# Kernel tuning notes

Measured on AMD Instinct MI355X. Metric: run time of the kernel, lower is better.

## Reference

```python
import jax, jax.numpy as jnp
import numpy as np

B, F, U, O, A, H = 8192, 1024, 512, 3, 6, 4  # batch, features, nb_units, nb_opponents, actions, heads
HD = U // H  # head dim


def setup_inputs() -> dict:
    key = jax.random.key(0)
    ks = jax.random.split(key, 12)
    s = 0.02
    rn = lambda k, shape: jax.random.normal(k, shape, jnp.float32) * s
    return {
        "features": jax.random.normal(ks[0], (B, F), jnp.float32),
        # agent latent Linear
        "W_al": rn(ks[1], (U, F)), "b_al": jnp.zeros((U,), jnp.float32),
        # MultiheadAttention in_proj (q,k,v stacked) and out_proj
        "W_in": rn(ks[2], (3 * U, U)), "b_in": jnp.zeros((3 * U,), jnp.float32),
        "W_out": rn(ks[3], (U, U)), "b_out": jnp.zeros((U,), jnp.float32),
        # agent head / policy / value
        "W_ah": rn(ks[4], (U, 2 * U)), "b_ah": jnp.zeros((U,), jnp.float32),
        "W_ap": rn(ks[5], (A, U)), "b_ap": jnp.zeros((A,), jnp.float32),
        "W_av": rn(ks[6], (1, U)), "b_av": jnp.zeros((1,), jnp.float32),
        # per-opponent stacks: latent, head, policy, value
        "W_ol": rn(ks[7], (O, U, F)), "b_ol": jnp.zeros((O, U), jnp.float32),
        "W_oh": rn(ks[8], (O, U, U)), "b_oh": jnp.zeros((O, U), jnp.float32),
        "W_op": rn(ks[9], (O, A, U)), "b_op": jnp.zeros((O, A), jnp.float32),
        "W_ov": rn(ks[10], (O, 1, U)), "b_ov": jnp.zeros((O, 1), jnp.float32),
    }


def reference(features, W_al, b_al, W_in, b_in, W_out, b_out, W_ah, b_ah,
              W_ap, b_ap, W_av, b_av, W_ol, b_ol, W_oh, b_oh, W_op, b_op, W_ov, b_ov):
    elu = jax.nn.elu
    # agent + per-opponent latents (per-opponent linears as one grouped GEMM)
    agent_latent = elu(features @ W_al.T + b_al)                                # [B,U]
    opp_lat = elu(jnp.einsum('bf,ouf->obu', features, W_ol) + b_ol[:, None, :])  # [O,B,U]

    # torch.nn.MultiheadAttention: query=[1,B,U] (agent), key=value=[O,B,U] (opponents)
    Wq, Wk, Wv = W_in[:U], W_in[U:2 * U], W_in[2 * U:]
    bq, bk, bv = b_in[:U], b_in[U:2 * U], b_in[2 * U:]
    q = (agent_latent @ Wq.T + bq).reshape(B, H, HD) * (1.0 / np.sqrt(HD))      # [B,H,HD]
    k = (jnp.einsum('obu,vu->obv', opp_lat, Wk) + bk).reshape(O, B, H, HD)
    v = (jnp.einsum('obu,vu->obv', opp_lat, Wv) + bv).reshape(O, B, H, HD)
    scores = jnp.einsum('bhd,obhd->bho', q, k)                                  # [B,H,O]
    w = jax.nn.softmax(scores, axis=-1)
    attn = jnp.einsum('bho,obhd->bhd', w, v).reshape(B, U)
    attn_out = attn @ W_out.T + b_out                                           # [B,U]
    opponents_influences = w.mean(axis=1)                                       # [B,O] (avg over heads)

    # agent head / policy / value
    cat = jnp.concatenate([agent_latent, attn_out], axis=1)                     # [B,2U]
    agent_head = elu(cat @ W_ah.T + b_ah)
    agent_policy = agent_head @ W_ap.T + b_ap                                   # [B,A]
    agent_value = agent_head @ W_av.T + b_av                                    # [B,1]

    # per-opponent head / policy / value (grouped GEMMs)
    opp_heads = elu(jnp.einsum('obu,ovu->obv', opp_lat, W_oh) + b_oh[:, None, :])  # [O,B,U]
    opponents_policies = jnp.einsum('obu,oau->boa', opp_heads, W_op) + b_op[None]   # [B,O,A]
    opponents_values = jnp.einsum('obu,ocu->boc', opp_heads, W_ov) + b_ov[None]     # [B,O,1]

    return (agent_policy, agent_value, opponents_policies, opponents_values, opponents_influences)
```

## Files before the change

kernel.cpp:

```cpp
#include <hip/hip_runtime.h>

typedef unsigned short u16;
typedef __bf16 bf16x8 __attribute__((ext_vector_type(8)));
typedef float f32x4 __attribute__((ext_vector_type(4)));

#define Bsz 8192
#define Fdim 1024
#define Udim 512
#define Odim 3
#define Adim 6
#define Hdim 4

#define OFF_FEAT   0
#define OFF_WAL    8388608
#define OFF_WIN    10485760
#define OFF_WOUT   11272192
#define OFF_WAH    11534336
#define OFF_WOH    12058624
#define OFF_LAT    12845056
#define OFF_Q      29622272
#define OFF_KV     33816576
#define OFF_OPH    67371008
#define OFF_WOUTT  79953920
#define OFF_WCOMB  80216064
#define OFF_BAHC   80478208
#define OFF_ZB     80479232

#define OUT_AP 0
#define OUT_AV 49152
#define OUT_OP 57344
#define OUT_OV 204800
#define OUT_IN 229376

__device__ __forceinline__ u16 f2bf(float f) {
  return __builtin_bit_cast(u16, (__bf16)f);
}
__device__ __forceinline__ float bf2f(u16 u) {
  return (float)__builtin_bit_cast(__bf16, u);
}

__device__ __forceinline__ void gload16(const u16* g, u16* s) {
  __builtin_amdgcn_global_load_lds(
      (const __attribute__((address_space(1))) unsigned int*)g,
      (__attribute__((address_space(3))) unsigned int*)s, 16, 0, 0);
}

#define CV_E0 2097152
#define CV_E1 2228224
#define CV_E2 2621440
#define CV_E3 2818048
#define CV_E4 2883584
#define CV_E5 3014656
#define CV_E6 3211264
__global__ __launch_bounds__(256) void convert_all(
    const float* __restrict__ f, const float* __restrict__ wal,
    const float* __restrict__ wol, const float* __restrict__ win,
    const float* __restrict__ wout, const float* __restrict__ wah,
    const float* __restrict__ woh, u16* __restrict__ dst,
    u16* __restrict__ woutT, float* __restrict__ bahc,
    const float* __restrict__ bout_f, const float* __restrict__ bah_f,
    float* __restrict__ zb) {
  if (blockIdx.x >= 12608) {
    const int wave = threadIdx.x >> 6, lane = threadIdx.x & 63;
    const int jbase = (blockIdx.x - 12608) * 8 + wave * 2;
#pragma unroll
    for (int t = 0; t < 2; ++t) {
      const int j = jbase + t;
      float s = 0.f;
#pragma unroll
      for (int c = 0; c < 8; ++c)
        s += wah[j * 1024 + 512 + c * 64 + lane] * bout_f[c * 64 + lane];
#pragma unroll
      for (int d = 32; d; d >>= 1) s += __shfl_xor(s, d, 64);
      if (lane == 0) bahc[j] = bah_f[j] + s;
    }
    return;
  }
  if (blockIdx.x >= 12544) {
    const int bid = blockIdx.x - 12544;
    if (bid == 0) {
      zb[threadIdx.x] = 0.f;
      zb[threadIdx.x + 256] = 0.f;
    }
    __shared__ float tile[64][65];
    const int bx = bid & 7, byy = bid >> 3;
    const int v0 = byy * 64, u0 = bx * 64;
#pragma unroll
    for (int it = 0; it < 16; ++it) {
      int idx = it * 256 + threadIdx.x;
      int r = idx >> 6, c = idx & 63;
      tile[r][c] = wout[(v0 + r) * 512 + u0 + c];
    }
    __syncthreads();
#pragma unroll
    for (int it = 0; it < 16; ++it) {
      int idx = it * 256 + threadIdx.x;
      int r = idx >> 6, c = idx & 63;
      woutT[(u0 + r) * 512 + v0 + c] = f2bf(tile[c][r]);
    }
    return;
  }
  int i = blockIdx.x * 256 + threadIdx.x;
  const float* src;
  int base;
  if (i < CV_E0)      { src = f;    base = 0; }
  else if (i < CV_E1) { src = wal;  base = CV_E0; }
  else if (i < CV_E2) { src = wol;  base = CV_E1; }
  else if (i < CV_E3) { src = win;  base = CV_E2; }
  else if (i < CV_E4) { src = wout; base = CV_E3; }
  else if (i < CV_E5) { src = wah;  base = CV_E4; }
  else                { src = woh;  base = CV_E5; }
  float4 v = ((const float4*)src)[i - base];
  ushort4 o;
  o.x = f2bf(v.x); o.y = f2bf(v.y); o.z = f2bf(v.z); o.w = f2bf(v.w);
  ((ushort4*)dst)[i] = o;
}

#define BAR() __builtin_amdgcn_s_barrier()
#define FENCE() asm volatile("" ::: "memory")
#define LGKM0() asm volatile("s_waitcnt lgkmcnt(0)" ::: "memory")
#define VMW(n) asm volatile("s_waitcnt vmcnt(" #n ")" ::: "memory")
#define MFMA(a, b, c) __builtin_amdgcn_mfma_f32_16x16x32_bf16(a, b, c, 0, 0, 0)
#define STAGE(MAT, SRC, LD, buf, ks, kb) do {                    \
    const u16* _s = (SRC) + (size_t)(kb) + (ks) * 32;            \
    gload16(_s, &MAT[buf][ks][wave * 512]);                      \
    gload16(_s + (size_t)128 * (LD), &MAT[buf][ks][4096 + wave * 512]); \
  } while (0)
#define RD_A(cur, ks, mh) do {                                   \
    _Pragma("unroll")                                            \
    for (int mi = 0; mi < 4; mi++)                               \
      a0[mi] = *(const bf16x8*)&As[cur][ks][aoff + (mh)*2048 + mi*512]; \
  } while (0)
#define RD_B(cur, ks) do {                                       \
    _Pragma("unroll")                                            \
    for (int ni = 0; ni < 4; ni++)                               \
      b0[ni] = *(const bf16x8*)&Bs[cur][ks][boff + ni*512];      \
  } while (0)
#define MFMA8(mh) do {                                           \
    __builtin_amdgcn_s_setprio(1);                               \
    _Pragma("unroll")                                            \
    for (int mi = 0; mi < 4; mi++) {                             \
      _Pragma("unroll")                                          \
      for (int ni = 0; ni < 4; ni++)                             \
        acc[(mh)*4+mi][ni] = MFMA(a0[mi], b0[ni], acc[(mh)*4+mi][ni]); \
    }                                                            \
    __builtin_amdgcn_s_setprio(0);                               \
  } while (0)

template <bool ELU>
__global__ __launch_bounds__(512, 2) void gemm256(
    const u16* __restrict__ A, const u16* __restrict__ Bw, u16* __restrict__ C,
    const float* __restrict__ bias1, const float* __restrict__ bias2,
    int bsplit, int K, int lda, int ldb, int ldc,
    long sAz, long sBz, long sCz, int sbz, float scale) {
  __shared__ __align__(16) u16 As[2][2][8192];
  __shared__ __align__(16) u16 Bs[2][2][8192];
  const int tid = threadIdx.x;
  const int wave = tid >> 6, lane = tid & 63;
  const int wr = wave >> 2, wc = wave & 3;

  const int nx = gridDim.x, ny = gridDim.y;
  const int nxy = nx * ny;
  const int nwg = nxy * gridDim.z;
  const int orig = blockIdx.x + nx * (blockIdx.y + ny * blockIdx.z);
  const int xcd = orig & 7;
  const int qd = nwg >> 3, rd = nwg & 7;
  const int wg = (xcd < rd ? xcd * (qd + 1) : rd * (qd + 1) + (xcd - rd) * qd)
               + (orig >> 3);
  const int z = wg / nxy;
  const int rem = wg - z * nxy;
  const int by = rem / nx;
  const int bx = rem - by * nx;

  A += (size_t)z * sAz;
  Bw += (size_t)z * sBz;
  C += (size_t)z * sCz;
  bias1 += (size_t)z * sbz;

  const int tM = by * 256, tN = bx * 256;

  const int srow = tid >> 2;
  const int schunk = ((tid & 3) ^ ((tid >> 3) & 3)) * 8;
  const u16* Asrc = A + (size_t)(tM + srow) * lda + schunk;
  const u16* Bsrc = Bw + (size_t)(tN + srow) * ldb + schunk;

  const int laneLo = lane & 15;
  const int pc8 = (((lane >> 4) ^ ((lane >> 1) & 3))) * 8;
  const int aoff = (wr * 128 + laneLo) * 32 + pc8;
  const int boff = (wc * 64 + laneLo) * 32 + pc8;

  f32x4 acc[8][4];
#pragma unroll
  for (int mi = 0; mi < 8; mi++)
#pragma unroll
    for (int ni = 0; ni < 4; ni++) acc[mi][ni] = (f32x4){0.f, 0.f, 0.f, 0.f};

  const int NT = K >> 6;

  STAGE(As, Asrc, lda, 0, 0, 0);
  STAGE(Bs, Bsrc, ldb, 0, 0, 0);
  STAGE(As, Asrc, lda, 0, 1, 0);
  STAGE(Bs, Bsrc, ldb, 0, 1, 0);
  VMW(4);
  BAR();

  int cur = 0;
  int kb = 64;
  bf16x8 a0[4], b0[4];
  for (int t = 0; t < NT; ++t) {
    const int nxt = cur ^ 1;
    const bool st = (t + 1 < NT);
    RD_B(cur, 0);
    RD_A(cur, 0, 0);
    if (st) STAGE(As, Asrc, lda, nxt, 0, kb);
    FENCE(); BAR(); LGKM0();
    MFMA8(0);
    FENCE(); BAR();
    RD_A(cur, 0, 1);
    if (st) STAGE(Bs, Bsrc, ldb, nxt, 0, kb);
    FENCE(); BAR(); LGKM0();
    MFMA8(1);
    if (st) { VMW(4); } else { VMW(0); }
    BAR();
    RD_B(cur, 1);
    RD_A(cur, 1, 0);
    if (st) STAGE(As, Asrc, lda, nxt, 1, kb);
    FENCE(); BAR(); LGKM0();
    MFMA8(0);
    FENCE(); BAR();
    RD_A(cur, 1, 1);
    if (st) STAGE(Bs, Bsrc, ldb, nxt, 1, kb);
    FENCE(); BAR(); LGKM0();
    MFMA8(1);
    if (st) { VMW(4); BAR(); }
    cur = nxt;
    kb += 64;
  }

#pragma unroll
  for (int ni = 0; ni < 4; ni++) {
    const int col = tN + wc * 64 + ni * 16 + laneLo;
    const float bv = (col < bsplit) ? bias1[col] : bias2[col - bsplit];
#pragma unroll
    for (int gm = 0; gm < 8; gm++) {
      const int row0 = tM + wr * 128 + gm * 16 + (lane >> 4) * 4;
#pragma unroll
      for (int r = 0; r < 4; r++) {
        float v = (acc[gm][ni][r] + bv) * scale;
        if (ELU) v = v > 0.f ? v : (__expf(v) - 1.f);
        C[(size_t)(row0 + r) * ldc + col] = f2bf(v);
      }
    }
  }
}
#undef STAGE
#undef RD_A
#undef RD_B
#undef MFMA8

__global__ __launch_bounds__(256) void mega(
    const u16* __restrict__ lat, const u16* __restrict__ win,
    const u16* __restrict__ woh, const u16* __restrict__ wahb,
    const u16* __restrict__ woutT,
    u16* __restrict__ qb, u16* __restrict__ kvb, u16* __restrict__ oph,
    u16* __restrict__ wcomb,
    const float* __restrict__ b_in, const float* __restrict__ b_oh,
    const float* __restrict__ zb) {
  constexpr int BM = 128, BK = 32, BN = 128, NI = 4;
  __shared__ __align__(16) u16 As[BM * BK];
  __shared__ __align__(16) u16 Bs[BN * BK];
  const int wave = threadIdx.x >> 6, lane = threadIdx.x & 63;

  const int orig = blockIdx.x;
  const int wg = (orig & 7) * 322 + (orig >> 3);

  const u16 *A, *Bw;
  u16* C;
  const float* bias;
  int bx, by, ldc, lda = 2048;
  bool elu = false;
  float scale = 1.f;
  if (wg < 256) {
    bx = wg & 3; by = wg >> 2;
    A = lat; Bw = win; C = qb; bias = b_in;
    ldc = 512; scale = 0.08838834764831845f;
  } else if (wg < 1792) {
    int t = wg - 256, o = t >> 9, r = t & 511;
    bx = r & 7; by = r >> 3;
    A = lat + 512 * (o + 1); Bw = win + 262144;
    C = kvb + (size_t)o * 8388608; bias = b_in + 512;
    ldc = 1024;
  } else if (wg < 2560) {
    int t = wg - 1792, o = t >> 8, r = t & 255;
    bx = r & 3; by = r >> 2;
    A = lat + 512 * (o + 1); Bw = woh + (size_t)o * 262144;
    C = oph + (size_t)o * 4194304; bias = b_oh + o * 512;
    ldc = 512; elu = true;
  } else {
    int t = wg - 2560;
    bx = t & 3; by = t >> 2;
    A = wahb + 512; lda = 1024; Bw = woutT;
    C = wcomb; bias = zb;
    ldc = 512;
  }
  const int tM = by * BM, tN = bx * BN;
  const int wr = wave >> 1, wc = wave & 1;

  f32x4 acc[4][NI];
#pragma unroll
  for (int i = 0; i < 4; i++)
#pragma unroll
    for (int j = 0; j < NI; j++) acc[i][j] = (f32x4){0.f, 0.f, 0.f, 0.f};

  const int srow = lane >> 2;
  const int scol = (lane & 3) * 8;

  for (int k0 = 0; k0 < 512; k0 += BK) {
    __syncthreads();
#pragma unroll
    for (int i = 0; i < 2; ++i) {
      int r = wave * 32 + i * 16;
      gload16(A + (size_t)(tM + r + srow) * lda + k0 + scol, &As[r * BK]);
    }
#pragma unroll
    for (int i = 0; i < 2; ++i) {
      int r = (wave * 2 + i) * 16;
      gload16(Bw + (size_t)(tN + r + srow) * 512 + k0 + scol, &Bs[r * BK]);
    }
    __syncthreads();
    bf16x8 af[4], bfr[NI];
#pragma unroll
    for (int mi = 0; mi < 4; mi++)
      af[mi] = *(const bf16x8*)&As[(wr * 64 + mi * 16 + (lane & 15)) * BK + (lane >> 4) * 8];
#pragma unroll
    for (int ni = 0; ni < NI; ni++)
      bfr[ni] = *(const bf16x8*)&Bs[(wc * 64 + ni * 16 + (lane & 15)) * BK + (lane >> 4) * 8];
#pragma unroll
    for (int mi = 0; mi < 4; mi++)
#pragma unroll
      for (int ni = 0; ni < NI; ni++)
        acc[mi][ni] = __builtin_amdgcn_mfma_f32_16x16x32_bf16(af[mi], bfr[ni], acc[mi][ni], 0, 0, 0);
  }

#pragma unroll
  for (int ni = 0; ni < NI; ni++) {
    int col = tN + wc * 64 + ni * 16 + (lane & 15);
    float bv = bias[col];
#pragma unroll
    for (int mi = 0; mi < 4; mi++) {
      int row0 = tM + wr * 64 + mi * 16 + (lane >> 4) * 4;
#pragma unroll
      for (int r = 0; r < 4; r++) {
        float v = (acc[mi][ni][r] + bv) * scale;
        if (elu) v = v > 0.f ? v : (__expf(v) - 1.f);
        C[(size_t)(row0 + r) * ldc + col] = f2bf(v);
      }
    }
  }
}

__global__ __launch_bounds__(512) void tail(
    const u16* __restrict__ lat, const u16* __restrict__ qb,
    const u16* __restrict__ kvb, const u16* __restrict__ wahb,
    const u16* __restrict__ wcomb, const float* __restrict__ bahc,
    const u16* __restrict__ oph,
    const float* __restrict__ Wap, const float* __restrict__ bap,
    const float* __restrict__ Wav, const float* __restrict__ bav,
    const float* __restrict__ Wop, const float* __restrict__ bop,
    const float* __restrict__ Wov, const float* __restrict__ bov,
    float* __restrict__ out) {
  __shared__ __align__(16) u16 AL[16384];
  __shared__ __align__(16) u16 ATT[16384];
  __shared__ __align__(16) u16 Bs[16384];
  const int tid = threadIdx.x;
  const int wave = tid >> 6, lane = tid & 63;
  const int row0 = blockIdx.x * 32;

#pragma unroll
  for (int j = 0; j < 4; ++j) {
    int gq = j * 512 + tid;
    int r = gq >> 6, s = gq & 63, c = s ^ (r & 7);
    gload16(lat + (size_t)(row0 + r) * 2048 + c * 8, &AL[j * 4096 + wave * 512]);
  }

  for (int t = 0; t < 4; ++t) {
    const int b = row0 + wave * 4 + t;
    const int rl = b - row0;
    const size_t qoff = (size_t)b * 512;
    float wacc0 = 0.f, wacc1 = 0.f, wacc2 = 0.f;
#pragma unroll
    for (int h = 0; h < 4; ++h) {
      const int off = h * 128 + lane * 2;
      ushort2 qu = *(const ushort2*)(qb + qoff + off);
      float qx = bf2f(qu.x), qy = bf2f(qu.y);
      float s[3];
#pragma unroll
      for (int o = 0; o < 3; ++o) {
        ushort2 ku = *(const ushort2*)(kvb + (size_t)o * (Bsz * 1024) + (size_t)b * 1024 + off);
        float p = qx * bf2f(ku.x) + qy * bf2f(ku.y);
#pragma unroll
        for (int d = 32; d; d >>= 1) p += __shfl_xor(p, d, 64);
        s[o] = p;
      }
      float m = fmaxf(s[0], fmaxf(s[1], s[2]));
      float e0 = __expf(s[0] - m), e1 = __expf(s[1] - m), e2 = __expf(s[2] - m);
      float inv = 1.f / (e0 + e1 + e2);
      float w0 = e0 * inv, w1 = e1 * inv, w2 = e2 * inv;
      wacc0 += w0; wacc1 += w1; wacc2 += w2;
      float ax = 0.f, ay = 0.f;
#pragma unroll
      for (int o = 0; o < 3; ++o) {
        float w = (o == 0) ? w0 : (o == 1) ? w1 : w2;
        ushort2 vu = *(const ushort2*)(kvb + (size_t)o * (Bsz * 1024) + (size_t)b * 1024 + 512 + off);
        ax += w * bf2f(vu.x);
        ay += w * bf2f(vu.y);
      }
      ushort2 st; st.x = f2bf(ax); st.y = f2bf(ay);
      const int col = off;
      const int slot = (col >> 3) ^ (rl & 7);
      *(ushort2*)(&ATT[rl * 512 + slot * 8 + (col & 7)]) = st;
    }
    if (lane == 0) {
      out[OUT_IN + (size_t)b * 3 + 0] = wacc0 * 0.25f;
      out[OUT_IN + (size_t)b * 3 + 1] = wacc1 * 0.25f;
      out[OUT_IN + (size_t)b * 3 + 2] = wacc2 * 0.25f;
    }
  }
  __syncthreads();

  const int ll = lane & 15, lh = lane >> 4, l7 = lane & 7;
  const int wc0 = wave * 64;
  f32x4 acc[2][4];
#pragma unroll
  for (int mf = 0; mf < 2; ++mf)
#pragma unroll
    for (int nf = 0; nf < 4; ++nf) acc[mf][nf] = (f32x4){0.f, 0.f, 0.f, 0.f};

  for (int step = 0; step < 32; ++step) {
    const u16* bsrc;
    int ldb;
    if (step < 16) { bsrc = wahb + step * 32;          ldb = 1024; }
    else           { bsrc = wcomb + (step - 16) * 32;  ldb = 512; }
    __syncthreads();
#pragma unroll
    for (int j = 0; j < 4; ++j) {
      int id = j * 512 + tid;
      gload16(bsrc + (size_t)(id >> 2) * ldb + (id & 3) * 8,
              &Bs[j * 4096 + wave * 512]);
    }
    __syncthreads();
    const u16* ABUF = (step < 16) ? AL : ATT;
    const int c9 = step & 15;
    bf16x8 a0 = *(const bf16x8*)&ABUF[ll * 512 + (((c9 * 4 + lh) ^ l7) * 8)];
    bf16x8 a1 = *(const bf16x8*)&ABUF[(16 + ll) * 512 + (((c9 * 4 + lh) ^ l7) * 8)];
#pragma unroll
    for (int nf = 0; nf < 4; ++nf) {
      bf16x8 bf = *(const bf16x8*)&Bs[(wc0 + nf * 16 + ll) * 32 + lh * 8];
      acc[0][nf] = __builtin_amdgcn_mfma_f32_16x16x32_bf16(a0, bf, acc[0][nf], 0, 0, 0);
      acc[1][nf] = __builtin_amdgcn_mfma_f32_16x16x32_bf16(a1, bf, acc[1][nf], 0, 0, 0);
    }
  }

#pragma unroll
  for (int nf = 0; nf < 4; ++nf) {
    const int col = wc0 + nf * 16 + ll;
    const float bb = bahc[col];
#pragma unroll
    for (int mf = 0; mf < 2; ++mf)
#pragma unroll
      for (int r = 0; r < 4; ++r) {
        const int row = mf * 16 + lh * 4 + r;
        float v = acc[mf][nf][r] + bb;
        v = v > 0.f ? v : (__expf(v) - 1.f);
        AL[row * 512 + (((col >> 3) ^ (row & 7)) * 8) + (col & 7)] = f2bf(v);
      }
  }
  __syncthreads();

  if (wave < 4) {
    const int rl = wave * 8 + (lane >> 3), kq = lane & 7;
    const int b = row0 + rl;
    bf16x8 av[8];
#pragma unroll
    for (int c = 0; c < 8; ++c)
      av[c] = *(const bf16x8*)&AL[rl * 512 + (((c * 8 + kq) ^ (rl & 7)) * 8)];
#pragma unroll
    for (int p = 0; p < 7; ++p) {
      const float* wg = (p < 6) ? Wap + p * 512 : Wav;
      float ac = 0.f;
#pragma unroll
      for (int c = 0; c < 8; ++c) {
        float4 w0 = *(const float4*)(wg + c * 64 + kq * 8);
        float4 w1 = *(const float4*)(wg + c * 64 + kq * 8 + 4);
        ac += (float)av[c][0] * w0.x + (float)av[c][1] * w0.y
            + (float)av[c][2] * w0.z + (float)av[c][3] * w0.w
            + (float)av[c][4] * w1.x + (float)av[c][5] * w1.y
            + (float)av[c][6] * w1.z + (float)av[c][7] * w1.w;
      }
      ac += __shfl_xor(ac, 1, 64);
      ac += __shfl_xor(ac, 2, 64);
      ac += __shfl_xor(ac, 4, 64);
      if (kq == p) {
        if (p < 6) out[OUT_AP + b * 6 + p] = ac + bap[p];
        else       out[OUT_AV + b] = ac + bav[0];
      }
    }
    for (int o = 0; o < 3; ++o) {
      const u16* src = oph + ((size_t)o * Bsz + b) * 512;
#pragma unroll
      for (int c = 0; c < 8; ++c)
        av[c] = *(const bf16x8*)(src + c * 64 + kq * 8);
#pragma unroll
      for (int p = 0; p < 7; ++p) {
        const float* wg = (p < 6) ? Wop + o * 3072 + p * 512 : Wov + o * 512;
        float ac = 0.f;
#pragma unroll
        for (int c = 0; c < 8; ++c) {
          float4 w0 = *(const float4*)(wg + c * 64 + kq * 8);
          float4 w1 = *(const float4*)(wg + c * 64 + kq * 8 + 4);
          ac += (float)av[c][0] * w0.x + (float)av[c][1] * w0.y
              + (float)av[c][2] * w0.z + (float)av[c][3] * w0.w
              + (float)av[c][4] * w1.x + (float)av[c][5] * w1.y
              + (float)av[c][6] * w1.z + (float)av[c][7] * w1.w;
        }
        ac += __shfl_xor(ac, 1, 64);
        ac += __shfl_xor(ac, 2, 64);
        ac += __shfl_xor(ac, 4, 64);
        if (kq == p) {
          if (p < 6) out[OUT_OP + b * 18 + o * 6 + p] = ac + bop[o * 6 + p];
          else       out[OUT_OV + b * 3 + o] = ac + bov[o];
        }
      }
    }
  }
}

extern "C" void kernel_launch(void* const* d_in, const int* in_sizes, int n_in,
                              void* d_out, int out_size, void* d_ws, size_t ws_size,
                              hipStream_t stream) {
  (void)in_sizes; (void)n_in; (void)out_size; (void)ws_size;
  const float* f     = (const float*)d_in[0];
  const float* W_al  = (const float*)d_in[1];
  const float* b_al  = (const float*)d_in[2];
  const float* W_in  = (const float*)d_in[3];
  const float* b_in  = (const float*)d_in[4];
  const float* W_out = (const float*)d_in[5];
  const float* b_out = (const float*)d_in[6];
  const float* W_ah  = (const float*)d_in[7];
  const float* b_ah  = (const float*)d_in[8];
  const float* W_ap  = (const float*)d_in[9];
  const float* b_ap  = (const float*)d_in[10];
  const float* W_av  = (const float*)d_in[11];
  const float* b_av  = (const float*)d_in[12];
  const float* W_ol  = (const float*)d_in[13];
  const float* b_ol  = (const float*)d_in[14];
  const float* W_oh  = (const float*)d_in[15];
  const float* b_oh  = (const float*)d_in[16];
  const float* W_op  = (const float*)d_in[17];
  const float* b_op  = (const float*)d_in[18];
  const float* W_ov  = (const float*)d_in[19];
  const float* b_ov  = (const float*)d_in[20];
  float* out = (float*)d_out;
  u16* ws = (u16*)d_ws;

  u16* feat  = ws + OFF_FEAT;
  u16* wal   = ws + OFF_WAL;
  u16* win   = ws + OFF_WIN;
  u16* wahb  = ws + OFF_WAH;
  u16* woh   = ws + OFF_WOH;
  u16* lat   = ws + OFF_LAT;
  u16* qbuf  = ws + OFF_Q;
  u16* kvb   = ws + OFF_KV;
  u16* oph   = ws + OFF_OPH;
  u16* woutT = ws + OFF_WOUTT;
  u16* wcomb = ws + OFF_WCOMB;
  float* bahc = (float*)(ws + OFF_BAHC);
  float* zb   = (float*)(ws + OFF_ZB);

  convert_all<<<12672, 256, 0, stream>>>(f, W_al, W_ol, W_in, W_out, W_ah,
                                         W_oh, ws, woutT, bahc, b_out, b_ah,
                                         zb);

  gemm256<true><<<dim3(8, 32, 1), 512, 0, stream>>>(
      feat, wal, lat, b_al, b_ol, 512, 1024, 1024, 1024, 2048, 0, 0, 0, 0, 1.f);

  mega<<<2576, 256, 0, stream>>>(
      lat, win, woh, wahb, woutT, qbuf, kvb, oph, wcomb, b_in, b_oh, zb);

  tail<<<256, 512, 0, stream>>>(lat, qbuf, kvb, wahb, wcomb, bahc, oph,
                                W_ap, b_ap, W_av, b_av,
                                W_op, b_op, W_ov, b_ov, out);
}
```

Measured before the change: 291.4 us.

## Double-buffer LDS tiles and XOR-swizzle columns in mega GEMM kernel

The mega GEMM kernel's shared-memory tiles become double-buffered, so the global-to-LDS loads for the next K step are issued before the MFMAs on the current buffer, with a single wait and barrier per iteration. The column offset used for staging and fragment reads is XOR-swizzled by row to reduce LDS bank conflicts. This doubles the LDS footprint, which may lower occupancy, and depends on the swizzle producing the same K ordering for A and B fragments.

```diff
diff --git a/kernel.cpp b/kernel.cpp
--- a/kernel.cpp
+++ b/kernel.cpp
@@ -267,8 +267,8 @@
     const float* __restrict__ b_in, const float* __restrict__ b_oh,
     const float* __restrict__ zb) {
   constexpr int BM = 128, BK = 32, BN = 128, NI = 4;
-  __shared__ __align__(16) u16 As[BM * BK];
-  __shared__ __align__(16) u16 Bs[BN * BK];
+  __shared__ __align__(16) u16 As[2][BM * BK];
+  __shared__ __align__(16) u16 Bs[2][BN * BK];
   const int wave = threadIdx.x >> 6, lane = threadIdx.x & 63;
 
   const int orig = blockIdx.x;
@@ -313,34 +313,50 @@
     for (int j = 0; j < NI; j++) acc[i][j] = (f32x4){0.f, 0.f, 0.f, 0.f};
 
   const int srow = lane >> 2;
-  const int scol = (lane & 3) * 8;
-
-  for (int k0 = 0; k0 < 512; k0 += BK) {
-    __syncthreads();
-#pragma unroll
-    for (int i = 0; i < 2; ++i) {
-      int r = wave * 32 + i * 16;
-      gload16(A + (size_t)(tM + r + srow) * lda + k0 + scol, &As[r * BK]);
-    }
-#pragma unroll
-    for (int i = 0; i < 2; ++i) {
-      int r = (wave * 2 + i) * 16;
-      gload16(Bw + (size_t)(tN + r + srow) * 512 + k0 + scol, &Bs[r * BK]);
-    }
-    __syncthreads();
+  const int scol = ((lane & 3) ^ ((lane >> 3) & 3)) * 8;
+  const int pc8 = ((lane >> 4) ^ ((lane >> 1) & 3)) * 8;
+
+#define MSTAGE(buf, k0) do {                                               \
+    _Pragma("unroll")                                                      \
+    for (int i = 0; i < 2; ++i) {                                          \
+      int r = wave * 32 + i * 16;                                          \
+      gload16(A + (size_t)(tM + r + srow) * lda + (k0) + scol,             \
+              &As[buf][r * BK]);                                           \
+    }                                                                      \
+    _Pragma("unroll")                                                      \
+    for (int i = 0; i < 2; ++i) {                                          \
+      int r = (wave * 2 + i) * 16;                                         \
+      gload16(Bw + (size_t)(tN + r + srow) * 512 + (k0) + scol,            \
+              &Bs[buf][r * BK]);                                           \
+    }                                                                      \
+  } while (0)
+
+  MSTAGE(0, 0);
+  VMW(0);
+  BAR();
+
+  int cur = 0;
+  for (int t = 0; t < 16; ++t) {
+    const int nxt = cur ^ 1;
+    if (t < 15) MSTAGE(nxt, (t + 1) * 32);
     bf16x8 af[4], bfr[NI];
 #pragma unroll
     for (int mi = 0; mi < 4; mi++)
-      af[mi] = *(const bf16x8*)&As[(wr * 64 + mi * 16 + (lane & 15)) * BK + (lane >> 4) * 8];
+      af[mi] = *(const bf16x8*)&As[cur][(wr * 64 + mi * 16 + (lane & 15)) * BK + pc8];
 #pragma unroll
     for (int ni = 0; ni < NI; ni++)
-      bfr[ni] = *(const bf16x8*)&Bs[(wc * 64 + ni * 16 + (lane & 15)) * BK + (lane >> 4) * 8];
+      bfr[ni] = *(const bf16x8*)&Bs[cur][(wc * 64 + ni * 16 + (lane & 15)) * BK + pc8];
 #pragma unroll
     for (int mi = 0; mi < 4; mi++)
 #pragma unroll
       for (int ni = 0; ni < NI; ni++)
         acc[mi][ni] = __builtin_amdgcn_mfma_f32_16x16x32_bf16(af[mi], bfr[ni], acc[mi][ni], 0, 0, 0);
-  }
+    FENCE();
+    VMW(0);
+    BAR();
+    cur = nxt;
+  }
+#undef MSTAGE
 
 #pragma unroll
   for (int ni = 0; ni < NI; ni++) {
```

Result: no change. 294.6 us, median of 2 (+1.1%).
